# Optimization experiments

Measured on AMD Instinct MI355X. Metric: run time of the kernel, lower is better.

Reference implementation:

```python
import jax, jax.numpy as jnp
import numpy as np

N_U = 50000
N_I = 50000
E = 800000
E_LBL = 200000
D_IN = 128
HID = 256
OUT = 128


def setup_inputs() -> dict:
    key = jax.random.key(0)
    ks = jax.random.split(key, 32)
    def glorot(k, shp):
        fan = shp[0] + shp[1]
        return jax.random.uniform(k, shp, jnp.float32, -1.0, 1.0) * np.sqrt(6.0 / fan)
    inp = {
        'x_user': jax.random.normal(ks[0], (N_U, D_IN), jnp.float32),
        'x_item': jax.random.normal(ks[1], (N_I, D_IN), jnp.float32),
        'edge_ui': jax.random.randint(ks[2], (2, E), 0, N_U, jnp.int32),
        'edge_iu': jax.random.randint(ks[3], (2, E), 0, N_I, jnp.int32),
        'edge_lbl': jax.random.randint(ks[4], (2, E_LBL), 0, N_U, jnp.int32),
        # layer 0 SAGE params (src_dim=D_IN, dst_dim=D_IN)
        'w_msg_ui0': glorot(ks[5], (D_IN, HID)), 'b_ui0': jnp.zeros((HID,), jnp.float32), 'w_root_ui0': glorot(ks[6], (D_IN, HID)),
        'w_msg_iu0': glorot(ks[7], (D_IN, HID)), 'b_iu0': jnp.zeros((HID,), jnp.float32), 'w_root_iu0': glorot(ks[8], (D_IN, HID)),
        # layer 1 SAGE params (src_dim=HID, dst_dim=HID)
        'w_msg_ui1': glorot(ks[9], (HID, HID)), 'b_ui1': jnp.zeros((HID,), jnp.float32), 'w_root_ui1': glorot(ks[10], (HID, HID)),
        'w_msg_iu1': glorot(ks[11], (HID, HID)), 'b_iu1': jnp.zeros((HID,), jnp.float32), 'w_root_iu1': glorot(ks[12], (HID, HID)),
        # per-node-type output linears on JK concat (2*HID -> OUT)
        'w_lin_u': glorot(ks[13], (2 * HID, OUT)), 'b_lin_u': jnp.zeros((OUT,), jnp.float32),
        'w_lin_i': glorot(ks[14], (2 * HID, OUT)), 'b_lin_i': jnp.zeros((OUT,), jnp.float32),
    }
    return inp


def _sage(x_src, x_dst, edge, w_msg, b_msg, w_root):
    # PyG SAGEConv(aggr='mean'): lin_l(mean_{j in N(i)} x_src[j]) + lin_r(x_dst[i])
    src, dst = edge[0], edge[1]
    n_dst = x_dst.shape[0]
    agg = jax.ops.segment_sum(x_src[src], dst, num_segments=n_dst)          # [n_dst, d_src]
    cnt = jax.ops.segment_sum(jnp.ones((edge.shape[1],), x_src.dtype), dst, num_segments=n_dst)
    mean = agg / jnp.maximum(cnt, 1.0)[:, None]
    return mean @ w_msg + b_msg + x_dst @ w_root


def reference(x_user, x_item, edge_ui, edge_iu, edge_lbl,
              w_msg_ui0, b_ui0, w_root_ui0, w_msg_iu0, b_iu0, w_root_iu0,
              w_msg_ui1, b_ui1, w_root_ui1, w_msg_iu1, b_iu1, w_root_iu1,
              w_lin_u, b_lin_u, w_lin_i, b_lin_i):
    # ----- encode: 2 HeteroConv(SAGEConv) layers -----
    item0 = _sage(x_user, x_item, edge_ui, w_msg_ui0, b_ui0, w_root_ui0)    # user->item
    user0 = _sage(x_item, x_user, edge_iu, b_msg=b_iu0, w_msg=w_msg_iu0, x_src=None, x_dst=None, edge=None, w_root=None) if False else _sage(x_item, x_user, edge_iu, w_msg_iu0, b_iu0, w_root_iu0)  # item->user
    item1 = _sage(user0, item0, edge_ui, w_msg_ui1, b_ui1, w_root_ui1)
    user1 = _sage(item0, user0, edge_iu, w_msg_iu1, b_iu1, w_root_iu1)
    # ----- JumpingKnowledge 'cat' + per-node-type linear -----
    z_user = jnp.concatenate([user0, user1], axis=-1) @ w_lin_u + b_lin_u   # [N_U, OUT]
    z_item = jnp.concatenate([item0, item1], axis=-1) @ w_lin_i + b_lin_i   # [N_I, OUT]
    # ----- decode: dot product over candidate edges (user, buys, item) -----
    pred = jnp.sum(z_user[edge_lbl[0]] * z_item[edge_lbl[1]], axis=-1)      # [E_LBL]
    return pred
```

## Files before the change

### kernel.cpp

```cpp
#include <hip/hip_runtime.h>

#define NU 50000
#define NI 50000
#define NE 800000
#define NLBL 200000
#define DIN 128
#define HID 256
#define DOUT 128

#define NSLICE 64
#define SLICE_SZ 12500
#define HALF_N 25000

typedef unsigned short ushort_t;
typedef __attribute__((ext_vector_type(8))) short bf16x8;
typedef __attribute__((ext_vector_type(4))) float f32x4;

__device__ __forceinline__ float bf2f(unsigned int u_shifted) {
    union { unsigned int i; float f; } v;
    v.i = u_shifted;
    return v.f;
}
__device__ __forceinline__ float bf_lo(unsigned int u) { return bf2f(u << 16); }
__device__ __forceinline__ float bf_hi(unsigned int u) { return bf2f(u & 0xffff0000u); }
__device__ __forceinline__ ushort_t f2bf(float f) {
    union { float f; unsigned int i; } v;
    v.f = f;
    unsigned int r = (v.i + 0x7FFFu + ((v.i >> 16) & 1u)) >> 16;
    return (ushort_t)r;
}
__device__ __forceinline__ void load_lds16(const ushort_t* g, ushort_t* s) {
    __builtin_amdgcn_global_load_lds(
        (const __attribute__((address_space(1))) void*)g,
        (__attribute__((address_space(3))) void*)s, 16, 0, 0);
}

#define CVT_PER 782
#define CVT_B (2 * CVT_PER)
#define SA_B 512

struct PrepArgs {
    const float* xu; ushort_t* xbu; const float* xi; ushort_t* xbi;
    const float *wm_ui1, *wr_ui1, *wm_iu1, *wr_iu1, *lin_i, *lin_u;
    float *G_i, *S_i, *G_u, *S_u;
};

__global__ __launch_bounds__(256) void prep_kernel(PrepArgs a) {
    int b = blockIdx.x;
    int t = threadIdx.x;
    if (b < CVT_B) {
        int cb = b;
        int which = (cb >= CVT_PER);
        if (which) cb -= CVT_PER;
        const float4* in = (const float4*)(which ? a.xi : a.xu);
        uint2* outp = (uint2*)(which ? a.xbi : a.xbu);
        const int n4 = NU * DIN / 4;
#pragma unroll
        for (int k = 0; k < 8; ++k) {
            int i = cb * 2048 + k * 256 + t;
            if (i < n4) {
                float4 v = in[i];
                uint2 o;
                o.x = (unsigned int)f2bf(v.x) | ((unsigned int)f2bf(v.y) << 16);
                o.y = (unsigned int)f2bf(v.z) | ((unsigned int)f2bf(v.w) << 16);
                outp[i] = o;
            }
        }
    } else {
        int r2 = b - CVT_B;
        int which = r2 >> 7;
        int e = (r2 & 127) * 256 + t;
        int k = e >> 7, n = e & 127;
        const float* W = (which == 0) ? a.wm_ui1 : (which == 1) ? a.wr_ui1
                       : (which == 2) ? a.wm_iu1 : a.wr_iu1;
        const float* L = (which < 2) ? a.lin_i : a.lin_u;
        float* O = (which == 0) ? a.G_i : (which == 1) ? a.S_i
                 : (which == 2) ? a.G_u : a.S_u;
        float s = (which & 1) ? L[k * 128 + n] : 0.f;
#pragma unroll 4
        for (int j = 0; j < HID; ++j) s += W[k * HID + j] * L[(HID + j) * 128 + n];
        O[k * 128 + n] = s;
    }
}

struct Prep2Args {
    const float *wm_ui0, *wr_ui0, *wm_iu0, *wr_iu0;
    const float *G_i, *S_i, *G_u, *S_u;
    const float *b_ui0, *b_iu0, *b_ui1, *b_iu1, *lin_i, *lin_u, *bl_i, *bl_u;
    ushort_t *VT1_i, *VT2_i, *VT3_i, *VT1_u, *VT2_u, *VT3_u;
    float *bz_i, *bz_u;
};

__global__ __launch_bounds__(256) void prep2_kernel(Prep2Args a) {
    int b = blockIdx.x, t = threadIdx.x;
    if (b < 384) {
        int v = b >> 6;
        int e = (b & 63) * 256 + t;
        int k = e >> 7, n = e & 127;
        const float *A1, *X1, *A2 = nullptr, *X2 = nullptr;
        ushort_t* O;
        switch (v) {
            case 0: A1 = a.wm_ui0; X1 = a.S_i; A2 = a.wr_iu0; X2 = a.G_i; O = a.VT1_i; break;
            case 1: A1 = a.wr_ui0; X1 = a.S_i; O = a.VT2_i; break;
            case 2: A1 = a.wm_iu0; X1 = a.G_i; O = a.VT3_i; break;
            case 3: A1 = a.wm_iu0; X1 = a.S_u; A2 = a.wr_ui0; X2 = a.G_u; O = a.VT1_u; break;
            case 4: A1 = a.wr_iu0; X1 = a.S_u; O = a.VT2_u; break;
            default: A1 = a.wm_ui0; X1 = a.G_u; O = a.VT3_u; break;
        }
        float s = 0.f;
#pragma unroll 4
        for (int j = 0; j < HID; ++j) s += A1[k * HID + j] * X1[j * 128 + n];
        if (A2) {
#pragma unroll 4
            for (int j = 0; j < HID; ++j) s += A2[k * HID + j] * X2[j * 128 + n];
        }
        O[n * 128 + k] = f2bf(s);
    } else {
        if (t >= 128) return;
        int user = b - 384;
        int n = t;
        const float* S = user ? a.S_u : a.S_i;
        const float* G = user ? a.G_u : a.G_i;
        const float* b_own0 = user ? a.b_iu0 : a.b_ui0;
        const float* b_oth0 = user ? a.b_ui0 : a.b_iu0;
        const float* b_own1 = user ? a.b_iu1 : a.b_ui1;
        const float* lin = user ? a.lin_u : a.lin_i;
        const float* bl = user ? a.bl_u : a.bl_i;
        float* o = user ? a.bz_u : a.bz_i;
        float s = bl[n];
        for (int j = 0; j < HID; ++j)
            s += b_own0[j] * S[j * 128 + n] + b_oth0[j] * G[j * 128 + n] +
                 b_own1[j] * lin[(HID + j) * 128 + n];
        o[n] = s;
    }
}

__global__ __launch_bounds__(256) void hist_lds(const int* __restrict__ dui,
                                                const int* __restrict__ diu,
                                                ushort_t* __restrict__ cnt_s) {
    __shared__ unsigned int cnt[HALF_N / 2];
    int b = blockIdx.x, t = threadIdx.x;
    int g = b >> 7, s = (b >> 1) & 63, half = b & 1;
    for (int i = t; i < HALF_N / 2; i += 256) cnt[i] = 0;
    __syncthreads();
    const int* dst = g ? diu : dui;
    int hbase = half * HALF_N;
    int e0 = s * SLICE_SZ;
    for (int i = e0 + t; i < e0 + SLICE_SZ; i += 256) {
        int d = dst[i] - hbase;
        if ((unsigned)d < (unsigned)HALF_N)
            atomicAdd(&cnt[d >> 1], 1u << ((d & 1) * 16));
    }
    __syncthreads();
    unsigned int* outp = (unsigned int*)(cnt_s + ((size_t)(g * NSLICE + s)) * 50000 + hbase);
    for (int i = t; i < HALF_N / 2; i += 256) outp[i] = cnt[i];
}

__global__ __launch_bounds__(256) void sscan(ushort_t* __restrict__ cnt_s, int* __restrict__ totals) {
    int idx = blockIdx.x * 256 + threadIdx.x;
    if (idx == 0) totals[100000] = 2 * NE;
    if (idx >= 100000) return;
    int g = idx / 50000, node = idx - g * 50000;
    size_t base = (size_t)g * NSLICE * 50000 + node;
    int run = 0;
#pragma unroll 4
    for (int s = 0; s < NSLICE; ++s) {
        size_t o = base + (size_t)s * 50000;
        int c = cnt_s[o];
        cnt_s[o] = (ushort_t)run;
        run += c;
    }
    totals[idx] = run;
}

__global__ __launch_bounds__(256) void scan1(const int* __restrict__ d, int* __restrict__ part, int n) {
    __shared__ int wsum[4];
    int b = blockIdx.x, t = threadIdx.x;
    int i0 = b * 2048 + t * 8;
    int s = 0;
#pragma unroll
    for (int k = 0; k < 8; ++k) s += (i0 + k < n) ? d[i0 + k] : 0;
#pragma unroll
    for (int off = 32; off > 0; off >>= 1) s += __shfl_down(s, off, 64);
    if ((t & 63) == 0) wsum[t >> 6] = s;
    __syncthreads();
    if (t == 0) part[b] = wsum[0] + wsum[1] + wsum[2] + wsum[3];
}

__global__ __launch_bounds__(256) void scan3(int* __restrict__ d, const int* __restrict__ part,
                                             int n, int nb) {
    __shared__ int wsum[4];
    __shared__ int blockoff_sh;
    int b = blockIdx.x, t = threadIdx.x;
    int lane = t & 63, wv = t >> 6;
    if (t < 64) {
        int v = (t < nb) ? part[t] : 0;
        int incl = v;
#pragma unroll
        for (int off = 1; off < 64; off <<= 1) {
            int tv = __shfl_up(incl, off, 64);
            if (t >= off) incl += tv;
        }
        if (t == b) blockoff_sh = incl - v;
    }
    int i0 = b * 2048 + t * 8;
    int v[8];
    int tsum = 0;
#pragma unroll
    for (int k = 0; k < 8; ++k) {
        v[k] = (i0 + k < n) ? d[i0 + k] : 0;
        tsum += v[k];
    }
    int incl = tsum;
#pragma unroll
    for (int off = 1; off < 64; off <<= 1) {
        int tv = __shfl_up(incl, off, 64);
        if (lane >= off) incl += tv;
    }
    if (lane == 63) wsum[wv] = incl;
    __syncthreads();
    int woff = 0;
    for (int w = 0; w < wv; ++w) woff += wsum[w];
    int run = blockoff_sh + woff + (incl - tsum);
#pragma unroll
    for (int k = 0; k < 8; ++k) {
        if (i0 + k < n) d[i0 + k] = run;
        run += v[k];
    }
}

__global__ __launch_bounds__(256) void fill_lds(const int* __restrict__ eui,
                                                const int* __restrict__ eiu,
                                                const ushort_t* __restrict__ cnt_s,
                                                const int* __restrict__ rowstart,
                                                ushort_t* __restrict__ csr) {
    __shared__ unsigned int off[HALF_N / 2];
    int b = blockIdx.x, t = threadIdx.x;
    int g = b >> 7, s = (b >> 1) & 63, half = b & 1;
    const unsigned int* st =
        (const unsigned int*)(cnt_s + ((size_t)(g * NSLICE + s)) * 50000 + half * HALF_N);
    for (int i = t; i < HALF_N / 2; i += 256) off[i] = st[i];
    __syncthreads();
    const int* src = g ? eiu : eui;
    const int* dst = src + NE;
    const int* rs = rowstart + g * 50000;
    int hbase = half * HALF_N;
    int e0 = s * SLICE_SZ;
    for (int i = e0 + t; i < e0 + SLICE_SZ; i += 256) {
        int dd = dst[i];
        int d = dd - hbase;
        if ((unsigned)d < (unsigned)HALF_N) {
            unsigned old = atomicAdd(&off[d >> 1], 1u << ((d & 1) * 16));
            int rel = (int)((old >> ((d & 1) * 16)) & 0xffffu);
            csr[(size_t)rs[dd] + rel] = (ushort_t)src[i];
        }
    }
}

struct AggJob { const int* sp; const ushort_t* csr; const ushort_t* x; ushort_t* out; int n; };
struct AggJobs2 { AggJob j[2]; };

__global__ __launch_bounds__(256) void agg_din(AggJobs2 js) {
    AggJob jb = js.j[blockIdx.y];
    int wave = (int)((blockIdx.x * 256u + threadIdx.x) >> 6);
    int lane = threadIdx.x & 63;
    const int l = lane & 31;
    const int h = lane >> 5;
    int w2 = wave * 2;
    if (w2 >= jb.n) return;
    int w = w2 + h;
    int s0 = jb.sp[w];
    int s1 = jb.sp[w + 1];
    int cnt = s1 - s0;
    float sc = (cnt > 0) ? 1.0f / (float)cnt : 0.0f;
    int cother = __shfl_xor(cnt, 32, 64);
    int cmax = (cnt > cother) ? cnt : cother;
    const uint2* xp = (const uint2*)jb.x;
    float f0 = 0.f, f1 = 0.f, f2 = 0.f, f3 = 0.f;
    float g0 = 0.f, g1 = 0.f, g2 = 0.f, g3 = 0.f;
    for (int chunk = 0; chunk < cmax; chunk += 32) {
        int mh = cnt - chunk;
        int safe = (mh > 0) ? ((l < mh) ? l : mh - 1) : 0;
        int vidx = (int)jb.csr[s0 + chunk + safe];
        int mm = cmax - chunk;
        if (mm > 32) mm = 32;
        int j = 0;
        for (; j + 3 < mm; j += 4) {
            int i0 = __shfl(vidx, j, 32);
            int i1 = __shfl(vidx, j + 1, 32);
            int i2 = __shfl(vidx, j + 2, 32);
            int i3 = __shfl(vidx, j + 3, 32);
            float m0 = (j < mh) ? 1.f : 0.f;
            float m1 = (j + 1 < mh) ? 1.f : 0.f;
            float m2 = (j + 2 < mh) ? 1.f : 0.f;
            float m3 = (j + 3 < mh) ? 1.f : 0.f;
            uint2 u0 = xp[(size_t)((j < mh) ? i0 : 0) * 32 + l];
            uint2 u1 = xp[(size_t)((j + 1 < mh) ? i1 : 0) * 32 + l];
            uint2 u2 = xp[(size_t)((j + 2 < mh) ? i2 : 0) * 32 + l];
            uint2 u3 = xp[(size_t)((j + 3 < mh) ? i3 : 0) * 32 + l];
            f0 = fmaf(m0, bf_lo(u0.x), f0); f1 = fmaf(m0, bf_hi(u0.x), f1);
            f2 = fmaf(m0, bf_lo(u0.y), f2); f3 = fmaf(m0, bf_hi(u0.y), f3);
            g0 = fmaf(m1, bf_lo(u1.x), g0); g1 = fmaf(m1, bf_hi(u1.x), g1);
            g2 = fmaf(m1, bf_lo(u1.y), g2); g3 = fmaf(m1, bf_hi(u1.y), g3);
            f0 = fmaf(m2, bf_lo(u2.x), f0); f1 = fmaf(m2, bf_hi(u2.x), f1);
            f2 = fmaf(m2, bf_lo(u2.y), f2); f3 = fmaf(m2, bf_hi(u2.y), f3);
            g0 = fmaf(m3, bf_lo(u3.x), g0); g1 = fmaf(m3, bf_hi(u3.x), g1);
            g2 = fmaf(m3, bf_lo(u3.y), g2); g3 = fmaf(m3, bf_hi(u3.y), g3);
        }
        for (; j < mm; ++j) {
            int i0 = __shfl(vidx, j, 32);
            float m0 = (j < mh) ? 1.f : 0.f;
            uint2 u0 = xp[(size_t)((j < mh) ? i0 : 0) * 32 + l];
            f0 = fmaf(m0, bf_lo(u0.x), f0); f1 = fmaf(m0, bf_hi(u0.x), f1);
            f2 = fmaf(m0, bf_lo(u0.y), f2); f3 = fmaf(m0, bf_hi(u0.y), f3);
        }
    }
    uint2 o;
    o.x = (unsigned int)f2bf((f0 + g0) * sc) | ((unsigned int)f2bf((f1 + g1) * sc) << 16);
    o.y = (unsigned int)f2bf((f2 + g2) * sc) | ((unsigned int)f2bf((f3 + g3) * sc) << 16);
    ((uint2*)jb.out)[(size_t)w * 32 + l] = o;
}

struct GemmJob {
    const ushort_t* A[3];
    const ushort_t* WT[3];
    int K[3];
    const float* bias;
    void* C;
};
struct GemmJobs2 { GemmJob j[2]; };

template <int NP, typename OutT>
__global__ __launch_bounds__(256) void gemmN(GemmJobs2 js, int M, int N) {
    GemmJob jb = js.j[blockIdx.z];
    __shared__ ushort_t sA[128 * 32];
    __shared__ ushort_t sB[128 * 32];
    const int tid = threadIdx.x;
    const int lane = tid & 63;
    const int wv = tid >> 6;
    const int wm = wv & 1, wn = wv >> 1;
    const int bm = blockIdx.y * 128, bn = blockIdx.x * 128;

    f32x4 acc[4][4] = {};

    const int srow = tid >> 2;
    const int scol = (tid & 3) * 8;

#pragma unroll
    for (int part = 0; part < NP; ++part) {
        const ushort_t* A = jb.A[part];
        const ushort_t* WT = jb.WT[part];
        const int K = jb.K[part];
        int ar0 = bm + srow;       if (ar0 > M - 1) ar0 = M - 1;
        int ar1 = bm + 64 + srow;  if (ar1 > M - 1) ar1 = M - 1;
        const size_t aoff0 = (size_t)ar0 * K + scol;
        const size_t aoff1 = (size_t)ar1 * K + scol;
        const size_t boff0 = (size_t)(bn + srow) * K + scol;
        const size_t boff1 = (size_t)(bn + 64 + srow) * K + scol;
        for (int k0 = 0; k0 < K; k0 += 32) {
            __syncthreads();
            load_lds16(A + aoff0 + k0, sA + tid * 8);
            load_lds16(A + aoff1 + k0, sA + 2048 + tid * 8);
            load_lds16(WT + boff0 + k0, sB + tid * 8);
            load_lds16(WT + boff1 + k0, sB + 2048 + tid * 8);
            __syncthreads();
            const ushort_t* pA = sA + ((wm * 64 + (lane & 15)) * 32 + (lane >> 4) * 8);
            const ushort_t* pB = sB + ((wn * 64 + (lane & 15)) * 32 + (lane >> 4) * 8);
            bf16x8 af[4], bfr[4];
#pragma unroll
            for (int mt = 0; mt < 4; ++mt) af[mt] = *(const bf16x8*)(pA + mt * 512);
#pragma unroll
            for (int nt = 0; nt < 4; ++nt) bfr[nt] = *(const bf16x8*)(pB + nt * 512);
#pragma unroll
            for (int mt = 0; mt < 4; ++mt)
#pragma unroll
                for (int nt = 0; nt < 4; ++nt)
                    acc[mt][nt] = __builtin_amdgcn_mfma_f32_16x16x32_bf16(
                        af[mt], bfr[nt], acc[mt][nt], 0, 0, 0);
        }
    }

#pragma unroll
    for (int mt = 0; mt < 4; ++mt) {
#pragma unroll
        for (int r = 0; r < 4; ++r) {
            int row = bm + wm * 64 + mt * 16 + (lane >> 4) * 4 + r;
            if (row >= M) continue;
#pragma unroll
            for (int nt = 0; nt < 4; ++nt) {
                int col = bn + wn * 64 + nt * 16 + (lane & 15);
                float v = acc[mt][nt][r] + jb.bias[col];
                if constexpr (sizeof(OutT) == 2)
                    ((ushort_t*)jb.C)[(size_t)row * N + col] = f2bf(v);
                else
                    ((float*)jb.C)[(size_t)row * N + col] = v;
            }
        }
    }
}

__global__ void decode_kernel(const int* __restrict__ lbl, const ushort_t* __restrict__ zu,
                              const ushort_t* __restrict__ zi, float* __restrict__ out, int n) {
    int gid = blockIdx.x * blockDim.x + threadIdx.x;
    int wave = gid >> 6;
    int lane = threadIdx.x & 63;
    int q = lane >> 4;
    int l = lane & 15;
    int e = wave * 4 + q;
    if (e >= n) return;
    int u = lbl[e];
    int it = lbl[n + e];
    uint4 a = ((const uint4*)zu)[(size_t)u * 16 + l];
    uint4 b = ((const uint4*)zi)[(size_t)it * 16 + l];
    float s = bf_lo(a.x) * bf_lo(b.x) + bf_hi(a.x) * bf_hi(b.x) +
              bf_lo(a.y) * bf_lo(b.y) + bf_hi(a.y) * bf_hi(b.y) +
              bf_lo(a.z) * bf_lo(b.z) + bf_hi(a.z) * bf_hi(b.z) +
              bf_lo(a.w) * bf_lo(b.w) + bf_hi(a.w) * bf_hi(b.w);
#pragma unroll
    for (int off = 8; off > 0; off >>= 1) s += __shfl_down(s, off, 16);
    if (l == 0) out[e] = s;
}

extern "C" void kernel_launch(void* const* d_in, const int* in_sizes, int n_in,
                              void* d_out, int out_size, void* d_ws, size_t ws_size,
                              hipStream_t stream) {
    const float* x_user = (const float*)d_in[0];
    const float* x_item = (const float*)d_in[1];
    const int* edge_ui = (const int*)d_in[2];
    const int* edge_iu = (const int*)d_in[3];
    const int* edge_lbl = (const int*)d_in[4];
    const float* w_msg_ui0 = (const float*)d_in[5];
    const float* b_ui0 = (const float*)d_in[6];
    const float* w_root_ui0 = (const float*)d_in[7];
    const float* w_msg_iu0 = (const float*)d_in[8];
    const float* b_iu0 = (const float*)d_in[9];
    const float* w_root_iu0 = (const float*)d_in[10];
    const float* w_msg_ui1 = (const float*)d_in[11];
    const float* b_ui1 = (const float*)d_in[12];
    const float* w_root_ui1 = (const float*)d_in[13];
    const float* w_msg_iu1 = (const float*)d_in[14];
    const float* b_iu1 = (const float*)d_in[15];
    const float* w_root_iu1 = (const float*)d_in[16];
    const float* w_lin_u = (const float*)d_in[17];
    const float* b_lin_u = (const float*)d_in[18];
    const float* w_lin_i = (const float*)d_in[19];
    const float* b_lin_i = (const float*)d_in[20];
    float* out = (float*)d_out;

    char* p = (char*)d_ws;
    ushort_t* user0 = (ushort_t*)p;  p += (size_t)NU * HID * 2;
    ushort_t* item0 = (ushort_t*)p;  p += (size_t)NI * HID * 2;
    ushort_t* user1 = (ushort_t*)p;  p += (size_t)NU * HID * 2;
    ushort_t* item1 = (ushort_t*)p;  p += (size_t)NI * HID * 2;
    (void)user0; (void)item0; (void)user1; (void)item1;
    ushort_t* A_i  = (ushort_t*)p;   p += (size_t)NI * DIN * 2;
    ushort_t* A_u  = (ushort_t*)p;   p += (size_t)NU * DIN * 2;
    ushort_t* B_i  = (ushort_t*)p;   p += (size_t)NI * DIN * 2;
    ushort_t* B_u  = (ushort_t*)p;   p += (size_t)NU * DIN * 2;
    ushort_t* xb_u  = (ushort_t*)p;  p += (size_t)NU * DIN * 2;
    ushort_t* xb_i  = (ushort_t*)p;  p += (size_t)NI * DIN * 2;
    ushort_t* z_user = (ushort_t*)p; p += (size_t)NU * DOUT * 2;
    ushort_t* z_item = (ushort_t*)p; p += (size_t)NI * DOUT * 2;
    int* totals     = (int*)p;       p += (size_t)(100000 + 64) * 4;
    ushort_t* csr   = (ushort_t*)p;  p += (size_t)2 * NE * 2;
    ushort_t* cnt_s = (ushort_t*)p;  p += (size_t)2 * NSLICE * 50000 * 2;
    int* scan_part  = (int*)p;       p += 64 * 4;
    float* G_i = (float*)p; p += (size_t)HID * 128 * 4;
    float* S_i = (float*)p; p += (size_t)HID * 128 * 4;
    float* G_u = (float*)p; p += (size_t)HID * 128 * 4;
    float* S_u = (float*)p; p += (size_t)HID * 128 * 4;
    ushort_t* VT1_i = (ushort_t*)p; p += (size_t)128 * 128 * 2;
    ushort_t* VT2_i = (ushort_t*)p; p += (size_t)128 * 128 * 2;
    ushort_t* VT3_i = (ushort_t*)p; p += (size_t)128 * 128 * 2;
    ushort_t* VT1_u = (ushort_t*)p; p += (size_t)128 * 128 * 2;
    ushort_t* VT2_u = (ushort_t*)p; p += (size_t)128 * 128 * 2;
    ushort_t* VT3_u = (ushort_t*)p; p += (size_t)128 * 128 * 2;
    float* bz_i = (float*)p; p += 128 * 4;
    float* bz_u = (float*)p; p += 128 * 4;

    const int NCNT = 100000;
    const int NB = (NCNT + 2047) / 2048;

    PrepArgs pa;
    pa.xu = x_user; pa.xbu = xb_u; pa.xi = x_item; pa.xbi = xb_i;
    pa.wm_ui1 = w_msg_ui1; pa.wr_ui1 = w_root_ui1;
    pa.wm_iu1 = w_msg_iu1; pa.wr_iu1 = w_root_iu1;
    pa.lin_i = w_lin_i; pa.lin_u = w_lin_u;
    pa.G_i = G_i; pa.S_i = S_i; pa.G_u = G_u; pa.S_u = S_u;
    prep_kernel<<<CVT_B + SA_B, 256, 0, stream>>>(pa);

    Prep2Args p2;
    p2.wm_ui0 = w_msg_ui0; p2.wr_ui0 = w_root_ui0;
    p2.wm_iu0 = w_msg_iu0; p2.wr_iu0 = w_root_iu0;
    p2.G_i = G_i; p2.S_i = S_i; p2.G_u = G_u; p2.S_u = S_u;
    p2.b_ui0 = b_ui0; p2.b_iu0 = b_iu0; p2.b_ui1 = b_ui1; p2.b_iu1 = b_iu1;
    p2.lin_i = w_lin_i; p2.lin_u = w_lin_u; p2.bl_i = b_lin_i; p2.bl_u = b_lin_u;
    p2.VT1_i = VT1_i; p2.VT2_i = VT2_i; p2.VT3_i = VT3_i;
    p2.VT1_u = VT1_u; p2.VT2_u = VT2_u; p2.VT3_u = VT3_u;
    p2.bz_i = bz_i; p2.bz_u = bz_u;
    prep2_kernel<<<386, 256, 0, stream>>>(p2);

    hist_lds<<<256, 256, 0, stream>>>(edge_ui + NE, edge_iu + NE, cnt_s);
    sscan<<<(NCNT + 255) / 256 + 1, 256, 0, stream>>>(cnt_s, totals);
    scan1<<<NB, 256, 0, stream>>>(totals, scan_part, NCNT);
    scan3<<<NB, 256, 0, stream>>>(totals, scan_part, NCNT, NB);
    fill_lds<<<256, 256, 0, stream>>>(edge_ui, edge_iu, cnt_s, totals, csr);

    {
        AggJobs2 aj = {{{totals, csr, xb_u, A_i, NI},
                        {totals + 50000, csr, xb_i, A_u, NU}}};
        agg_din<<<dim3((NI / 2 * 64) / 256, 2), 256, 0, stream>>>(aj);
    }
    {
        AggJobs2 aj = {{{totals, csr, A_u, B_i, NI},
                        {totals + 50000, csr, A_i, B_u, NU}}};
        agg_din<<<dim3((NI / 2 * 64) / 256, 2), 256, 0, stream>>>(aj);
    }

    {
        GemmJobs2 gj = {{{{A_i, xb_i, B_i}, {VT1_i, VT2_i, VT3_i}, {DIN, DIN, DIN}, bz_i, z_item},
                         {{A_u, xb_u, B_u}, {VT1_u, VT2_u, VT3_u}, {DIN, DIN, DIN}, bz_u, z_user}}};
        gemmN<3, ushort_t><<<dim3(DOUT / 128, (NU + 127) / 128, 2), 256, 0, stream>>>(gj, NU, DOUT);
    }

    decode_kernel<<<(((NLBL + 3) / 4) * 64 + 255) / 256, 256, 0, stream>>>(
        edge_lbl, z_user, z_item, out, NLBL);
}
```

Before: 398.3 us.

## Fuse prep, histogram, scan and CSR fill into one cooperative kernel; widen gather

Merges the seven preprocessing launches (bf16 conversion, weight folding, histogram, slice scan, block scans, CSR fill) into a single cooperative kernel of 256 blocks that uses grid syncs between phases, removing launch gaps. Separately, the mean-aggregation kernel now handles four nodes per wave with 16 lanes each loading 16-byte uint4 chunks instead of two nodes with 32 lanes loading 8 bytes. The fused kernel relies on all 256 blocks being co-resident with a large LDS array, and it serializes phases that previously had independent grid sizes.

```diff
diff --git a/kernel.cpp b/kernel.cpp
--- a/kernel.cpp
+++ b/kernel.cpp
@@ -1,4 +1,7 @@
 #include <hip/hip_runtime.h>
+#include <hip/hip_cooperative_groups.h>
+
+namespace cg = cooperative_groups;
 
 #define NU 50000
 #define NI 50000
@@ -39,17 +42,45 @@
 #define CVT_B (2 * CVT_PER)
 #define SA_B 512
 
-struct PrepArgs {
+struct MegaArgs {
     const float* xu; ushort_t* xbu; const float* xi; ushort_t* xbi;
     const float *wm_ui1, *wr_ui1, *wm_iu1, *wr_iu1, *lin_i, *lin_u;
     float *G_i, *S_i, *G_u, *S_u;
+    const float *wm_ui0, *wr_ui0, *wm_iu0, *wr_iu0;
+    const float *b_ui0, *b_iu0, *b_ui1, *b_iu1, *bl_i, *bl_u;
+    ushort_t *VT1_i, *VT2_i, *VT3_i, *VT1_u, *VT2_u, *VT3_u;
+    float *bz_i, *bz_u;
+    const int *eui, *eiu;
+    ushort_t* cnt_s;
+    int* totals;
+    int* scan_part;
+    ushort_t* csr;
 };
 
-__global__ __launch_bounds__(256) void prep_kernel(PrepArgs a) {
-    int b = blockIdx.x;
-    int t = threadIdx.x;
-    if (b < CVT_B) {
-        int cb = b;
+__global__ __launch_bounds__(256) void mega_kernel(MegaArgs a) {
+    cg::grid_group gg = cg::this_grid();
+    __shared__ unsigned int sh[HALF_N / 2];
+    const int b = blockIdx.x;
+    const int t = threadIdx.x;
+
+    {
+        int g = b >> 7, s = (b >> 1) & 63, half = b & 1;
+        for (int i = t; i < HALF_N / 2; i += 256) sh[i] = 0;
+        __syncthreads();
+        const int* dst = (g ? a.eiu : a.eui) + NE;
+        int hbase = half * HALF_N;
+        int e0 = s * SLICE_SZ;
+        for (int i = e0 + t; i < e0 + SLICE_SZ; i += 256) {
+            int d = dst[i] - hbase;
+            if ((unsigned)d < (unsigned)HALF_N)
+                atomicAdd(&sh[d >> 1], 1u << ((d & 1) * 16));
+        }
+        __syncthreads();
+        unsigned int* outp = (unsigned int*)(a.cnt_s + ((size_t)(g * NSLICE + s)) * 50000 + hbase);
+        for (int i = t; i < HALF_N / 2; i += 256) outp[i] = sh[i];
+    }
+    for (int task = b; task < CVT_B; task += 256) {
+        int cb = task;
         int which = (cb >= CVT_PER);
         if (which) cb -= CVT_PER;
         const float4* in = (const float4*)(which ? a.xi : a.xu);
@@ -66,10 +97,10 @@
                 outp[i] = o;
             }
         }
-    } else {
-        int r2 = b - CVT_B;
-        int which = r2 >> 7;
-        int e = (r2 & 127) * 256 + t;
+    }
+    for (int task = b; task < SA_B; task += 256) {
+        int which = task >> 7;
+        int e = (task & 127) * 256 + t;
         int k = e >> 7, n = e & 127;
         const float* W = (which == 0) ? a.wm_ui1 : (which == 1) ? a.wr_ui1
                        : (which == 2) ? a.wm_iu1 : a.wr_iu1;
@@ -81,178 +112,145 @@
         for (int j = 0; j < HID; ++j) s += W[k * HID + j] * L[(HID + j) * 128 + n];
         O[k * 128 + n] = s;
     }
-}
-
-struct Prep2Args {
-    const float *wm_ui0, *wr_ui0, *wm_iu0, *wr_iu0;
-    const float *G_i, *S_i, *G_u, *S_u;
-    const float *b_ui0, *b_iu0, *b_ui1, *b_iu1, *lin_i, *lin_u, *bl_i, *bl_u;
-    ushort_t *VT1_i, *VT2_i, *VT3_i, *VT1_u, *VT2_u, *VT3_u;
-    float *bz_i, *bz_u;
-};
-
-__global__ __launch_bounds__(256) void prep2_kernel(Prep2Args a) {
-    int b = blockIdx.x, t = threadIdx.x;
-    if (b < 384) {
-        int v = b >> 6;
-        int e = (b & 63) * 256 + t;
-        int k = e >> 7, n = e & 127;
-        const float *A1, *X1, *A2 = nullptr, *X2 = nullptr;
-        ushort_t* O;
-        switch (v) {
-            case 0: A1 = a.wm_ui0; X1 = a.S_i; A2 = a.wr_iu0; X2 = a.G_i; O = a.VT1_i; break;
-            case 1: A1 = a.wr_ui0; X1 = a.S_i; O = a.VT2_i; break;
-            case 2: A1 = a.wm_iu0; X1 = a.G_i; O = a.VT3_i; break;
-            case 3: A1 = a.wm_iu0; X1 = a.S_u; A2 = a.wr_ui0; X2 = a.G_u; O = a.VT1_u; break;
-            case 4: A1 = a.wr_iu0; X1 = a.S_u; O = a.VT2_u; break;
-            default: A1 = a.wm_ui0; X1 = a.G_u; O = a.VT3_u; break;
-        }
-        float s = 0.f;
+    gg.sync();
+
+    {
+        if (b == 0 && t == 0) a.totals[100000] = 2 * NE;
+#pragma unroll
+        for (int h = 0; h < 2; ++h) {
+            int idx = h * 65536 + b * 256 + t;
+            if (idx < 100000) {
+                int g = idx / 50000, node = idx - g * 50000;
+                size_t base = (size_t)g * NSLICE * 50000 + node;
+                int run = 0;
 #pragma unroll 4
-        for (int j = 0; j < HID; ++j) s += A1[k * HID + j] * X1[j * 128 + n];
-        if (A2) {
+                for (int s = 0; s < NSLICE; ++s) {
+                    size_t o = base + (size_t)s * 50000;
+                    int c = a.cnt_s[o];
+                    a.cnt_s[o] = (ushort_t)run;
+                    run += c;
+                }
+                a.totals[idx] = run;
+            }
+        }
+    }
+    for (int task = b; task < 386; task += 256) {
+        if (task < 384) {
+            int v = task >> 6;
+            int e = (task & 63) * 256 + t;
+            int k = e >> 7, n = e & 127;
+            const float *A1, *X1, *A2 = nullptr, *X2 = nullptr;
+            ushort_t* O;
+            switch (v) {
+                case 0: A1 = a.wm_ui0; X1 = a.S_i; A2 = a.wr_iu0; X2 = a.G_i; O = a.VT1_i; break;
+                case 1: A1 = a.wr_ui0; X1 = a.S_i; O = a.VT2_i; break;
+                case 2: A1 = a.wm_iu0; X1 = a.G_i; O = a.VT3_i; break;
+                case 3: A1 = a.wm_iu0; X1 = a.S_u; A2 = a.wr_ui0; X2 = a.G_u; O = a.VT1_u; break;
+                case 4: A1 = a.wr_iu0; X1 = a.S_u; O = a.VT2_u; break;
+                default: A1 = a.wm_ui0; X1 = a.G_u; O = a.VT3_u; break;
+            }
+            float s = 0.f;
 #pragma unroll 4
-            for (int j = 0; j < HID; ++j) s += A2[k * HID + j] * X2[j * 128 + n];
-        }
-        O[n * 128 + k] = f2bf(s);
-    } else {
-        if (t >= 128) return;
-        int user = b - 384;
-        int n = t;
-        const float* S = user ? a.S_u : a.S_i;
-        const float* G = user ? a.G_u : a.G_i;
-        const float* b_own0 = user ? a.b_iu0 : a.b_ui0;
-        const float* b_oth0 = user ? a.b_ui0 : a.b_iu0;
-        const float* b_own1 = user ? a.b_iu1 : a.b_ui1;
-        const float* lin = user ? a.lin_u : a.lin_i;
-        const float* bl = user ? a.bl_u : a.bl_i;
-        float* o = user ? a.bz_u : a.bz_i;
-        float s = bl[n];
-        for (int j = 0; j < HID; ++j)
-            s += b_own0[j] * S[j * 128 + n] + b_oth0[j] * G[j * 128 + n] +
-                 b_own1[j] * lin[(HID + j) * 128 + n];
-        o[n] = s;
-    }
-}
-
-__global__ __launch_bounds__(256) void hist_lds(const int* __restrict__ dui,
-                                                const int* __restrict__ diu,
-                                                ushort_t* __restrict__ cnt_s) {
-    __shared__ unsigned int cnt[HALF_N / 2];
-    int b = blockIdx.x, t = threadIdx.x;
-    int g = b >> 7, s = (b >> 1) & 63, half = b & 1;
-    for (int i = t; i < HALF_N / 2; i += 256) cnt[i] = 0;
-    __syncthreads();
-    const int* dst = g ? diu : dui;
-    int hbase = half * HALF_N;
-    int e0 = s * SLICE_SZ;
-    for (int i = e0 + t; i < e0 + SLICE_SZ; i += 256) {
-        int d = dst[i] - hbase;
-        if ((unsigned)d < (unsigned)HALF_N)
-            atomicAdd(&cnt[d >> 1], 1u << ((d & 1) * 16));
-    }
-    __syncthreads();
-    unsigned int* outp = (unsigned int*)(cnt_s + ((size_t)(g * NSLICE + s)) * 50000 + hbase);
-    for (int i = t; i < HALF_N / 2; i += 256) outp[i] = cnt[i];
-}
-
-__global__ __launch_bounds__(256) void sscan(ushort_t* __restrict__ cnt_s, int* __restrict__ totals) {
-    int idx = blockIdx.x * 256 + threadIdx.x;
-    if (idx == 0) totals[100000] = 2 * NE;
-    if (idx >= 100000) return;
-    int g = idx / 50000, node = idx - g * 50000;
-    size_t base = (size_t)g * NSLICE * 50000 + node;
-    int run = 0;
+            for (int j = 0; j < HID; ++j) s += A1[k * HID + j] * X1[j * 128 + n];
+            if (A2) {
 #pragma unroll 4
-    for (int s = 0; s < NSLICE; ++s) {
-        size_t o = base + (size_t)s * 50000;
-        int c = cnt_s[o];
-        cnt_s[o] = (ushort_t)run;
-        run += c;
-    }
-    totals[idx] = run;
-}
-
-__global__ __launch_bounds__(256) void scan1(const int* __restrict__ d, int* __restrict__ part, int n) {
-    __shared__ int wsum[4];
-    int b = blockIdx.x, t = threadIdx.x;
-    int i0 = b * 2048 + t * 8;
-    int s = 0;
-#pragma unroll
-    for (int k = 0; k < 8; ++k) s += (i0 + k < n) ? d[i0 + k] : 0;
-#pragma unroll
-    for (int off = 32; off > 0; off >>= 1) s += __shfl_down(s, off, 64);
-    if ((t & 63) == 0) wsum[t >> 6] = s;
-    __syncthreads();
-    if (t == 0) part[b] = wsum[0] + wsum[1] + wsum[2] + wsum[3];
-}
-
-__global__ __launch_bounds__(256) void scan3(int* __restrict__ d, const int* __restrict__ part,
-                                             int n, int nb) {
-    __shared__ int wsum[4];
-    __shared__ int blockoff_sh;
-    int b = blockIdx.x, t = threadIdx.x;
-    int lane = t & 63, wv = t >> 6;
-    if (t < 64) {
-        int v = (t < nb) ? part[t] : 0;
-        int incl = v;
+                for (int j = 0; j < HID; ++j) s += A2[k * HID + j] * X2[j * 128 + n];
+            }
+            O[n * 128 + k] = f2bf(s);
+        } else if (t < 128) {
+            int user = task - 384;
+            int n = t;
+            const float* S = user ? a.S_u : a.S_i;
+            const float* G = user ? a.G_u : a.G_i;
+            const float* b_own0 = user ? a.b_iu0 : a.b_ui0;
+            const float* b_oth0 = user ? a.b_ui0 : a.b_iu0;
+            const float* b_own1 = user ? a.b_iu1 : a.b_ui1;
+            const float* lin = user ? a.lin_u : a.lin_i;
+            const float* bl = user ? a.bl_u : a.bl_i;
+            float* o = user ? a.bz_u : a.bz_i;
+            float s = bl[n];
+            for (int j = 0; j < HID; ++j)
+                s += b_own0[j] * S[j * 128 + n] + b_oth0[j] * G[j * 128 + n] +
+                     b_own1[j] * lin[(HID + j) * 128 + n];
+            o[n] = s;
+        }
+    }
+    gg.sync();
+
+    if (b < 49) {
+        int* wsum = (int*)sh;
+        int i0 = b * 2048 + t * 8;
+        int s = 0;
+#pragma unroll
+        for (int k = 0; k < 8; ++k) s += (i0 + k < 100000) ? a.totals[i0 + k] : 0;
+#pragma unroll
+        for (int off = 32; off > 0; off >>= 1) s += __shfl_down(s, off, 64);
+        if ((t & 63) == 0) wsum[t >> 6] = s;
+        __syncthreads();
+        if (t == 0) a.scan_part[b] = wsum[0] + wsum[1] + wsum[2] + wsum[3];
+    }
+    gg.sync();
+
+    if (b < 49) {
+        int* wsum = (int*)sh;
+        int* blockoff_sh = (int*)(sh + 8);
+        int lane = t & 63, wv = t >> 6;
+        if (t < 64) {
+            int v = (t < 49) ? a.scan_part[t] : 0;
+            int incl = v;
+#pragma unroll
+            for (int off = 1; off < 64; off <<= 1) {
+                int tv = __shfl_up(incl, off, 64);
+                if (t >= off) incl += tv;
+            }
+            if (t == b) *blockoff_sh = incl - v;
+        }
+        int i0 = b * 2048 + t * 8;
+        int v[8];
+        int tsum = 0;
+#pragma unroll
+        for (int k = 0; k < 8; ++k) {
+            v[k] = (i0 + k < 100000) ? a.totals[i0 + k] : 0;
+            tsum += v[k];
+        }
+        int incl = tsum;
 #pragma unroll
         for (int off = 1; off < 64; off <<= 1) {
             int tv = __shfl_up(incl, off, 64);
-            if (t >= off) incl += tv;
-        }
-        if (t == b) blockoff_sh = incl - v;
-    }
-    int i0 = b * 2048 + t * 8;
-    int v[8];
-    int tsum = 0;
-#pragma unroll
-    for (int k = 0; k < 8; ++k) {
-        v[k] = (i0 + k < n) ? d[i0 + k] : 0;
-        tsum += v[k];
-    }
-    int incl = tsum;
-#pragma unroll
-    for (int off = 1; off < 64; off <<= 1) {
-        int tv = __shfl_up(incl, off, 64);
-        if (lane >= off) incl += tv;
-    }
-    if (lane == 63) wsum[wv] = incl;
-    __syncthreads();
-    int woff = 0;
-    for (int w = 0; w < wv; ++w) woff += wsum[w];
-    int run = blockoff_sh + woff + (incl - tsum);
-#pragma unroll
-    for (int k = 0; k < 8; ++k) {
-        if (i0 + k < n) d[i0 + k] = run;
-        run += v[k];
-    }
-}
-
-__global__ __launch_bounds__(256) void fill_lds(const int* __restrict__ eui,
-                                                const int* __restrict__ eiu,
-                                                const ushort_t* __restrict__ cnt_s,
-                                                const int* __restrict__ rowstart,
-                                                ushort_t* __restrict__ csr) {
-    __shared__ unsigned int off[HALF_N / 2];
-    int b = blockIdx.x, t = threadIdx.x;
-    int g = b >> 7, s = (b >> 1) & 63, half = b & 1;
-    const unsigned int* st =
-        (const unsigned int*)(cnt_s + ((size_t)(g * NSLICE + s)) * 50000 + half * HALF_N);
-    for (int i = t; i < HALF_N / 2; i += 256) off[i] = st[i];
-    __syncthreads();
-    const int* src = g ? eiu : eui;
-    const int* dst = src + NE;
-    const int* rs = rowstart + g * 50000;
-    int hbase = half * HALF_N;
-    int e0 = s * SLICE_SZ;
-    for (int i = e0 + t; i < e0 + SLICE_SZ; i += 256) {
-        int dd = dst[i];
-        int d = dd - hbase;
-        if ((unsigned)d < (unsigned)HALF_N) {
-            unsigned old = atomicAdd(&off[d >> 1], 1u << ((d & 1) * 16));
-            int rel = (int)((old >> ((d & 1) * 16)) & 0xffffu);
-            csr[(size_t)rs[dd] + rel] = (ushort_t)src[i];
+            if (lane >= off) incl += tv;
+        }
+        if (lane == 63) wsum[wv] = incl;
+        __syncthreads();
+        int woff = 0;
+        for (int w = 0; w < wv; ++w) woff += wsum[w];
+        int run = *blockoff_sh + woff + (incl - tsum);
+#pragma unroll
+        for (int k = 0; k < 8; ++k) {
+            if (i0 + k < 100000) a.totals[i0 + k] = run;
+            run += v[k];
+        }
+    }
+    gg.sync();
+
+    {
+        int g = b >> 7, s = (b >> 1) & 63, half = b & 1;
+        const unsigned int* st =
+            (const unsigned int*)(a.cnt_s + ((size_t)(g * NSLICE + s)) * 50000 + half * HALF_N);
+        for (int i = t; i < HALF_N / 2; i += 256) sh[i] = st[i];
+        __syncthreads();
+        const int* src = g ? a.eiu : a.eui;
+        const int* dst = src + NE;
+        const int* rs = a.totals + g * 50000;
+        int hbase = half * HALF_N;
+        int e0 = s * SLICE_SZ;
+        for (int i = e0 + t; i < e0 + SLICE_SZ; i += 256) {
+            int dd = dst[i];
+            int d = dd - hbase;
+            if ((unsigned)d < (unsigned)HALF_N) {
+                unsigned old = atomicAdd(&sh[d >> 1], 1u << ((d & 1) * 16));
+                int rel = (int)((old >> ((d & 1) * 16)) & 0xffffu);
+                a.csr[(size_t)rs[dd] + rel] = (ushort_t)src[i];
+            }
         }
     }
 }
@@ -264,61 +262,67 @@
     AggJob jb = js.j[blockIdx.y];
     int wave = (int)((blockIdx.x * 256u + threadIdx.x) >> 6);
     int lane = threadIdx.x & 63;
-    const int l = lane & 31;
-    const int h = lane >> 5;
-    int w2 = wave * 2;
-    if (w2 >= jb.n) return;
-    int w = w2 + h;
+    const int l = lane & 15;
+    const int h = lane >> 4;
+    int w4 = wave * 4;
+    if (w4 >= jb.n) return;
+    int w = w4 + h;
     int s0 = jb.sp[w];
     int s1 = jb.sp[w + 1];
     int cnt = s1 - s0;
     float sc = (cnt > 0) ? 1.0f / (float)cnt : 0.0f;
-    int cother = __shfl_xor(cnt, 32, 64);
-    int cmax = (cnt > cother) ? cnt : cother;
-    const uint2* xp = (const uint2*)jb.x;
+    int cmax = cnt;
+    {
+        int c1 = __shfl_xor(cmax, 16, 64); cmax = (cmax > c1) ? cmax : c1;
+        int c2 = __shfl_xor(cmax, 32, 64); cmax = (cmax > c2) ? cmax : c2;
+    }
+    const uint4* xp = (const uint4*)jb.x;
     float f0 = 0.f, f1 = 0.f, f2 = 0.f, f3 = 0.f;
-    float g0 = 0.f, g1 = 0.f, g2 = 0.f, g3 = 0.f;
-    for (int chunk = 0; chunk < cmax; chunk += 32) {
+    float f4 = 0.f, f5 = 0.f, f6 = 0.f, f7 = 0.f;
+#define ACC8(m, u)                                                     \
+    f0 = fmaf(m, bf_lo(u.x), f0); f1 = fmaf(m, bf_hi(u.x), f1);        \
+    f2 = fmaf(m, bf_lo(u.y), f2); f3 = fmaf(m, bf_hi(u.y), f3);        \
+    f4 = fmaf(m, bf_lo(u.z), f4); f5 = fmaf(m, bf_hi(u.z), f5);        \
+    f6 = fmaf(m, bf_lo(u.w), f6); f7 = fmaf(m, bf_hi(u.w), f7);
+    for (int chunk = 0; chunk < cmax; chunk += 16) {
         int mh = cnt - chunk;
         int safe = (mh > 0) ? ((l < mh) ? l : mh - 1) : 0;
         int vidx = (int)jb.csr[s0 + chunk + safe];
         int mm = cmax - chunk;
-        if (mm > 32) mm = 32;
+        if (mm > 16) mm = 16;
         int j = 0;
         for (; j + 3 < mm; j += 4) {
-            int i0 = __shfl(vidx, j, 32);
-            int i1 = __shfl(vidx, j + 1, 32);
-            int i2 = __shfl(vidx, j + 2, 32);
-            int i3 = __shfl(vidx, j + 3, 32);
+            int i0 = __shfl(vidx, j, 16);
+            int i1 = __shfl(vidx, j + 1, 16);
+            int i2 = __shfl(vidx, j + 2, 16);
+            int i3 = __shfl(vidx, j + 3, 16);
             float m0 = (j < mh) ? 1.f : 0.f;
             float m1 = (j + 1 < mh) ? 1.f : 0.f;
             float m2 = (j + 2 < mh) ? 1.f : 0.f;
             float m3 = (j + 3 < mh) ? 1.f : 0.f;
-            uint2 u0 = xp[(size_t)((j < mh) ? i0 : 0) * 32 + l];
-            uint2 u1 = xp[(size_t)((j + 1 < mh) ? i1 : 0) * 32 + l];
-            uint2 u2 = xp[(size_t)((j + 2 < mh) ? i2 : 0) * 32 + l];
-            uint2 u3 = xp[(size_t)((j + 3 < mh) ? i3 : 0) * 32 + l];
-            f0 = fmaf(m0, bf_lo(u0.x), f0); f1 = fmaf(m0, bf_hi(u0.x), f1);
-            f2 = fmaf(m0, bf_lo(u0.y), f2); f3 = fmaf(m0, bf_hi(u0.y), f3);
-            g0 = fmaf(m1, bf_lo(u1.x), g0); g1 = fmaf(m1, bf_hi(u1.x), g1);
-            g2 = fmaf(m1, bf_lo(u1.y), g2); g3 = fmaf(m1, bf_hi(u1.y), g3);
-            f0 = fmaf(m2, bf_lo(u2.x), f0); f1 = fmaf(m2, bf_hi(u2.x), f1);
-            f2 = fmaf(m2, bf_lo(u2.y), f2); f3 = fmaf(m2, bf_hi(u2.y), f3);
-            g0 = fmaf(m3, bf_lo(u3.x), g0); g1 = fmaf(m3, bf_hi(u3.x), g1);
-            g2 = fmaf(m3, bf_lo(u3.y), g2); g3 = fmaf(m3, bf_hi(u3.y), g3);
+            uint4 u0 = xp[(size_t)((j < mh) ? i0 : 0) * 16 + l];
+            uint4 u1 = xp[(size_t)((j + 1 < mh) ? i1 : 0) * 16 + l];
+            uint4 u2 = xp[(size_t)((j + 2 < mh) ? i2 : 0) * 16 + l];
+            uint4 u3 = xp[(size_t)((j + 3 < mh) ? i3 : 0) * 16 + l];
+            ACC8(m0, u0);
+            ACC8(m1, u1);
+            ACC8(m2, u2);
+            ACC8(m3, u3);
         }
         for (; j < mm; ++j) {
-            int i0 = __shfl(vidx, j, 32);
+            int i0 = __shfl(vidx, j, 16);
             float m0 = (j < mh) ? 1.f : 0.f;
-            uint2 u0 = xp[(size_t)((j < mh) ? i0 : 0) * 32 + l];
-            f0 = fmaf(m0, bf_lo(u0.x), f0); f1 = fmaf(m0, bf_hi(u0.x), f1);
-            f2 = fmaf(m0, bf_lo(u0.y), f2); f3 = fmaf(m0, bf_hi(u0.y), f3);
-        }
-    }
-    uint2 o;
-    o.x = (unsigned int)f2bf((f0 + g0) * sc) | ((unsigned int)f2bf((f1 + g1) * sc) << 16);
-    o.y = (unsigned int)f2bf((f2 + g2) * sc) | ((unsigned int)f2bf((f3 + g3) * sc) << 16);
-    ((uint2*)jb.out)[(size_t)w * 32 + l] = o;
+            uint4 u0 = xp[(size_t)((j < mh) ? i0 : 0) * 16 + l];
+            ACC8(m0, u0);
+        }
+    }
+#undef ACC8
+    uint4 o;
+    o.x = (unsigned int)f2bf(f0 * sc) | ((unsigned int)f2bf(f1 * sc) << 16);
+    o.y = (unsigned int)f2bf(f2 * sc) | ((unsigned int)f2bf(f3 * sc) << 16);
+    o.z = (unsigned int)f2bf(f4 * sc) | ((unsigned int)f2bf(f5 * sc) << 16);
+    o.w = (unsigned int)f2bf(f6 * sc) | ((unsigned int)f2bf(f7 * sc) << 16);
+    ((uint4*)jb.out)[(size_t)w * 16 + l] = o;
 }
 
 struct GemmJob {
@@ -478,43 +482,35 @@
     float* bz_i = (float*)p; p += 128 * 4;
     float* bz_u = (float*)p; p += 128 * 4;
 
-    const int NCNT = 100000;
-    const int NB = (NCNT + 2047) / 2048;
-
-    PrepArgs pa;
-    pa.xu = x_user; pa.xbu = xb_u; pa.xi = x_item; pa.xbi = xb_i;
-    pa.wm_ui1 = w_msg_ui1; pa.wr_ui1 = w_root_ui1;
-    pa.wm_iu1 = w_msg_iu1; pa.wr_iu1 = w_root_iu1;
-    pa.lin_i = w_lin_i; pa.lin_u = w_lin_u;
-    pa.G_i = G_i; pa.S_i = S_i; pa.G_u = G_u; pa.S_u = S_u;
-    prep_kernel<<<CVT_B + SA_B, 256, 0, stream>>>(pa);
-
-    Prep2Args p2;
-    p2.wm_ui0 = w_msg_ui0; p2.wr_ui0 = w_root_ui0;
-    p2.wm_iu0 = w_msg_iu0; p2.wr_iu0 = w_root_iu0;
-    p2.G_i = G_i; p2.S_i = S_i; p2.G_u = G_u; p2.S_u = S_u;
-    p2.b_ui0 = b_ui0; p2.b_iu0 = b_iu0; p2.b_ui1 = b_ui1; p2.b_iu1 = b_iu1;
-    p2.lin_i = w_lin_i; p2.lin_u = w_lin_u; p2.bl_i = b_lin_i; p2.bl_u = b_lin_u;
-    p2.VT1_i = VT1_i; p2.VT2_i = VT2_i; p2.VT3_i = VT3_i;
-    p2.VT1_u = VT1_u; p2.VT2_u = VT2_u; p2.VT3_u = VT3_u;
-    p2.bz_i = bz_i; p2.bz_u = bz_u;
-    prep2_kernel<<<386, 256, 0, stream>>>(p2);
-
-    hist_lds<<<256, 256, 0, stream>>>(edge_ui + NE, edge_iu + NE, cnt_s);
-    sscan<<<(NCNT + 255) / 256 + 1, 256, 0, stream>>>(cnt_s, totals);
-    scan1<<<NB, 256, 0, stream>>>(totals, scan_part, NCNT);
-    scan3<<<NB, 256, 0, stream>>>(totals, scan_part, NCNT, NB);
-    fill_lds<<<256, 256, 0, stream>>>(edge_ui, edge_iu, cnt_s, totals, csr);
+    MegaArgs ma;
+    ma.xu = x_user; ma.xbu = xb_u; ma.xi = x_item; ma.xbi = xb_i;
+    ma.wm_ui1 = w_msg_ui1; ma.wr_ui1 = w_root_ui1;
+    ma.wm_iu1 = w_msg_iu1; ma.wr_iu1 = w_root_iu1;
+    ma.lin_i = w_lin_i; ma.lin_u = w_lin_u;
+    ma.G_i = G_i; ma.S_i = S_i; ma.G_u = G_u; ma.S_u = S_u;
+    ma.wm_ui0 = w_msg_ui0; ma.wr_ui0 = w_root_ui0;
+    ma.wm_iu0 = w_msg_iu0; ma.wr_iu0 = w_root_iu0;
+    ma.b_ui0 = b_ui0; ma.b_iu0 = b_iu0; ma.b_ui1 = b_ui1; ma.b_iu1 = b_iu1;
+    ma.bl_i = b_lin_i; ma.bl_u = b_lin_u;
+    ma.VT1_i = VT1_i; ma.VT2_i = VT2_i; ma.VT3_i = VT3_i;
+    ma.VT1_u = VT1_u; ma.VT2_u = VT2_u; ma.VT3_u = VT3_u;
+    ma.bz_i = bz_i; ma.bz_u = bz_u;
+    ma.eui = edge_ui; ma.eiu = edge_iu;
+    ma.cnt_s = cnt_s; ma.totals = totals; ma.scan_part = scan_part; ma.csr = csr;
+    {
+        void* kargs[] = { &ma };
+        hipLaunchCooperativeKernel((void*)mega_kernel, dim3(256), dim3(256), kargs, 0, stream);
+    }
 
     {
         AggJobs2 aj = {{{totals, csr, xb_u, A_i, NI},
                         {totals + 50000, csr, xb_i, A_u, NU}}};
-        agg_din<<<dim3((NI / 2 * 64) / 256, 2), 256, 0, stream>>>(aj);
+        agg_din<<<dim3((NI / 4 * 64) / 256, 2), 256, 0, stream>>>(aj);
     }
     {
         AggJobs2 aj = {{{totals, csr, A_u, B_i, NI},
                         {totals + 50000, csr, A_i, B_u, NU}}};
-        agg_din<<<dim3((NI / 2 * 64) / 256, 2), 256, 0, stream>>>(aj);
+        agg_din<<<dim3((NI / 4 * 64) / 256, 2), 256, 0, stream>>>(aj);
     }
 
     {
```

Result: slower. 571.8 us (+43.5%).
